# Kernel tuning notes

Hardware: AMD Instinct MI355X
Metric: run time of the kernel (lower is better)

Reference implementation:

```python
import jax, jax.numpy as jnp
import numpy as np

N = 8192
D = 512


def setup_inputs() -> dict:
    key = jax.random.key(0)
    k_h, k_a, k_q, k_k, k_v = jax.random.split(key, 5)
    H = jax.random.normal(k_h, (N, D), dtype=jnp.float32)
    A = jax.random.uniform(k_a, (N, N), dtype=jnp.float32)
    W_Q = jax.random.uniform(k_q, (D, D), dtype=jnp.float32)
    W_K = jax.random.uniform(k_k, (D, D), dtype=jnp.float32)
    W_V = jax.random.uniform(k_v, (D, D), dtype=jnp.float32)
    return {"H": H, "A": A, "W_Q": W_Q, "W_K": W_K, "W_V": W_V}


def reference(H, A, W_Q, W_K, W_V):
    # Q = H @ W_Q, K = H @ W_K; scores = Q @ K^T  -> [N, N]
    scale = 1.0 / jnp.sqrt(jnp.asarray(H.shape[1], dtype=H.dtype))
    HQ = H @ W_Q                      # [N, D]
    HK = H @ W_K                      # [N, D]
    scores = jnp.einsum('nd,md->nm', HQ, HK)  # [N, N]
    scores = scores * A * scale       # elementwise adjacency mask + scale
    attn = jax.nn.softmax(scores, axis=1)
    return attn @ (H @ W_V)           # [N, D]
```

## Files before the change

### kernel.cpp

```cpp
#include <hip/hip_runtime.h>
#include <cmath>


typedef unsigned short u16;
typedef unsigned int   u32;
typedef float f32x4 __attribute__((ext_vector_type(4)));
typedef short s16x8 __attribute__((ext_vector_type(8)));

#define DEVI static __device__ __forceinline__

DEVI u16 f2bf(float x) { u32 u = __float_as_uint(x); u32 r = u + 0x7fffu + ((u >> 16) & 1u); return (u16)(r >> 16); }
DEVI float bf2f(u16 b) { return __uint_as_float((u32)b << 16); }

DEVI f32x4 mm_bf16(s16x8 a, s16x8 b, f32x4 c) {
  return __builtin_amdgcn_mfma_f32_16x16x32_bf16(a, b, c, 0, 0, 0);
}

DEVI uint4 scaleP(uint4 v, float f) {
  u32* w = (u32*)&v;
#pragma unroll
  for (int j = 0; j < 4; j++) {
    u32 lo = __float_as_uint(__uint_as_float(w[j] << 16) * f) + 0x8000u;
    u32 hi = __float_as_uint(__uint_as_float(w[j] & 0xffff0000u) * f) + 0x8000u;
    w[j] = __builtin_amdgcn_perm(hi, lo, 0x07060302);
  }
  return v;
}


__global__ void k_split(const float* __restrict__ X, u16* __restrict__ Xhi, u16* __restrict__ Xlo, int n4) {
  int i = blockIdx.x * 256 + threadIdx.x;
  if (i >= n4) return;
  float4 v = ((const float4*)X)[i];
  u16 h0 = f2bf(v.x), h1 = f2bf(v.y), h2 = f2bf(v.z), h3 = f2bf(v.w);
  u16 l0 = f2bf(v.x - bf2f(h0)), l1 = f2bf(v.y - bf2f(h1));
  u16 l2 = f2bf(v.z - bf2f(h2)), l3 = f2bf(v.w - bf2f(h3));
  ((uint2*)Xhi)[i] = make_uint2((u32)h0 | ((u32)h1 << 16), (u32)h2 | ((u32)h3 << 16));
  ((uint2*)Xlo)[i] = make_uint2((u32)l0 | ((u32)l1 << 16), (u32)l2 | ((u32)l3 << 16));
}

__global__ void k_prepW(const float* __restrict__ W0, const float* __restrict__ W1, const float* __restrict__ W2,
                        u16* __restrict__ Thi, u16* __restrict__ Tlo) {
  int idx = blockIdx.x * 256 + threadIdx.x;
  if (idx >= 3 * 512 * 512) return;
  int w = idx >> 18, n = (idx >> 9) & 511, k = idx & 511;
  const float* W = (w == 0) ? W0 : (w == 1) ? W1 : W2;
  float v = W[k * 512 + n];
  u16 h = f2bf(v);
  Thi[idx] = h;
  Tlo[idx] = f2bf(v - bf2f(h));
}

__global__ void k_transpose(const u16* __restrict__ in, u16* __restrict__ out, int R, int C) {
  __shared__ u16 t[64][72];
  const int rb = blockIdx.x * 64, cb = blockIdx.y * 64;
  const int r = threadIdx.x >> 2, c4 = (threadIdx.x & 3) * 16;
  const u16* src = in + (size_t)(rb + r) * C + cb + c4;
  *(uint4*)&t[r][c4] = *(const uint4*)src;
  *(uint4*)&t[r][c4 + 8] = *(const uint4*)(src + 8);
  __syncthreads();
  u16 v[16];
#pragma unroll
  for (int j = 0; j < 16; j++) v[j] = t[c4 + j][r];
  uint4 o0, o1;
  o0.x = v[0] | ((u32)v[1] << 16); o0.y = v[2] | ((u32)v[3] << 16);
  o0.z = v[4] | ((u32)v[5] << 16); o0.w = v[6] | ((u32)v[7] << 16);
  o1.x = v[8] | ((u32)v[9] << 16); o1.y = v[10] | ((u32)v[11] << 16);
  o1.z = v[12] | ((u32)v[13] << 16); o1.w = v[14] | ((u32)v[15] << 16);
  u16* dst = out + (size_t)(cb + r) * R + rb + c4;
  *(uint4*)dst = o0;
  *(uint4*)(dst + 8) = o1;
}


template<int EPI, int PASSES, int KSPLIT>
__launch_bounds__(256, 2)
__global__ void k_big(const u16* __restrict__ Ahi, const u16* __restrict__ Alo,
                      const u16* __restrict__ Bhi, const u16* __restrict__ Blo,
                      int M, int N, int K,
                      float* __restrict__ Cf, float* __restrict__ Cf1,
                      float* __restrict__ Cf2, float* __restrict__ Cf3,
                      const float* __restrict__ Adj, float* __restrict__ mC,
                      float* __restrict__ lC, u16* __restrict__ Pout,
                      const float* __restrict__ Fsc, float scale)
{
  constexpr int LDSU = (EPI == 2) ? 33792 : 15360;
  __shared__ __align__(16) u16 lds[LDSU];
  u16* sAh = lds;
  u16* sAl = lds + 10240;
  u16* sBh = lds + ((PASSES == 3) ? 20480 : 10240);
  u16* sBl = lds + 25600;

  const int tid = threadIdx.x, lane = tid & 63, wid = tid >> 6;
  const int wn = wid & 1, wm = wid >> 1;
  const int lr = lane & 15, lk = lane >> 4;
  const int mbase = blockIdx.x * 256, nbase = blockIdx.y * 128;
  const int srow = tid >> 1, shalf = tid & 1;
  const size_t Ks = (size_t)K;

  int kbeg = 0, kend = K;
  if constexpr (KSPLIT > 1) {
    const int steps = K >> 5, bz = blockIdx.z;
    kbeg = ((steps * bz) / KSPLIT) << 5;
    kend = ((steps * (bz + 1)) / KSPLIT) << 5;
  }

  f32x4 acc[8][4] = {};

  for (int kt = kbeg; kt < kend; kt += 32) {
    const size_t a0 = (size_t)(mbase + srow) * Ks + kt + shalf * 16;
    const size_t a1 = a0 + (size_t)128 * Ks;
    const size_t b0 = (size_t)(nbase + srow) * Ks + kt + shalf * 16;
    uint4 vah0 = *(const uint4*)(Ahi + a0), vah1 = *(const uint4*)(Ahi + a0 + 8);
    uint4 vah2 = *(const uint4*)(Ahi + a1), vah3 = *(const uint4*)(Ahi + a1 + 8);
    uint4 vbh0 = *(const uint4*)(Bhi + b0), vbh1 = *(const uint4*)(Bhi + b0 + 8);
    uint4 val0, val1, val2, val3, vbl0, vbl1;
    if constexpr (PASSES == 3) {
      val0 = *(const uint4*)(Alo + a0); val1 = *(const uint4*)(Alo + a0 + 8);
      val2 = *(const uint4*)(Alo + a1); val3 = *(const uint4*)(Alo + a1 + 8);
      vbl0 = *(const uint4*)(Blo + b0); vbl1 = *(const uint4*)(Blo + b0 + 8);
    }
    if constexpr (EPI == 3) {
      const float f0 = Fsc[((size_t)(kt >> 7) << 13) + mbase + srow];
      const float f1 = Fsc[((size_t)(kt >> 7) << 13) + mbase + 128 + srow];
      vah0 = scaleP(vah0, f0); vah1 = scaleP(vah1, f0);
      vah2 = scaleP(vah2, f1); vah3 = scaleP(vah3, f1);
    }
    __syncthreads();
    const int so = srow * 40 + shalf * 16;
    *(uint4*)(sAh + so) = vah0;        *(uint4*)(sAh + so + 8) = vah1;
    *(uint4*)(sAh + 5120 + so) = vah2; *(uint4*)(sAh + 5120 + so + 8) = vah3;
    *(uint4*)(sBh + so) = vbh0;        *(uint4*)(sBh + so + 8) = vbh1;
    if constexpr (PASSES == 3) {
      *(uint4*)(sAl + so) = val0;        *(uint4*)(sAl + so + 8) = val1;
      *(uint4*)(sAl + 5120 + so) = val2; *(uint4*)(sAl + 5120 + so + 8) = val3;
      *(uint4*)(sBl + so) = vbl0;        *(uint4*)(sBl + so + 8) = vbl1;
    }
    __syncthreads();

    s16x8 ah[8], al[8];
#pragma unroll
    for (int m = 0; m < 8; m++) {
      const int ro = (wm * 128 + m * 16 + lr) * 40 + lk * 8;
      ah[m] = *(const s16x8*)(sAh + ro);
      if constexpr (PASSES == 3) al[m] = *(const s16x8*)(sAl + ro);
    }
#pragma unroll
    for (int nt = 0; nt < 4; nt++) {
      const int ro = (wn * 64 + nt * 16 + lr) * 40 + lk * 8;
      s16x8 bh = *(const s16x8*)(sBh + ro);
#pragma unroll
      for (int m = 0; m < 8; m++) acc[m][nt] = mm_bf16(ah[m], bh, acc[m][nt]);
      if constexpr (PASSES == 3) {
        s16x8 bl = *(const s16x8*)(sBl + ro);
#pragma unroll
        for (int m = 0; m < 8; m++) acc[m][nt] = mm_bf16(ah[m], bl, acc[m][nt]);
#pragma unroll
        for (int m = 0; m < 8; m++) acc[m][nt] = mm_bf16(al[m], bh, acc[m][nt]);
      }
    }
  }

  if constexpr (EPI == 2) {
    const int c = blockIdx.x * 2 + wm;
#pragma unroll
    for (int nt = 0; nt < 4; nt++) {
      const int q_l = wn * 64 + nt * 16 + lr;
      const float* arow = Adj + (size_t)(nbase + q_l) * (size_t)M + mbase + wm * 128 + lk * 4;
      float4 a4[8];
#pragma unroll
      for (int mt = 0; mt < 8; mt++) a4[mt] = *(const float4*)(arow + mt * 16);
      float mx = -3.4e38f;
#pragma unroll
      for (int mt = 0; mt < 8; mt++)
#pragma unroll
        for (int r = 0; r < 4; r++) {
          float s = acc[mt][nt][r] * ((const float*)&a4[mt])[r] * scale;
          acc[mt][nt][r] = s;
          mx = fmaxf(mx, s);
        }
      mx = fmaxf(mx, __shfl_xor(mx, 16));
      mx = fmaxf(mx, __shfl_xor(mx, 32));
      float sm = 0.f;
#pragma unroll
      for (int mt = 0; mt < 8; mt++)
#pragma unroll
        for (int r = 0; r < 4; r++) {
          float p = __expf(acc[mt][nt][r] - mx);
          acc[mt][nt][r] = p;
          sm += p;
        }
      sm += __shfl_xor(sm, 16);
      sm += __shfl_xor(sm, 32);
      if (lane < 16) {
        mC[(size_t)c * N + nbase + wn * 64 + nt * 16 + lane] = mx;
        lC[(size_t)c * N + nbase + wn * 64 + nt * 16 + lane] = sm;
      }
    }
    __syncthreads();
    u16* pb = lds;
#pragma unroll
    for (int nt = 0; nt < 4; nt++) {
      const int q_l = wn * 64 + nt * 16 + lr;
#pragma unroll
      for (int mt = 0; mt < 8; mt++) {
        const int kvo = wm * 128 + mt * 16 + lk * 4;
        u32 u0 = (u32)f2bf(acc[mt][nt][0]) | ((u32)f2bf(acc[mt][nt][1]) << 16);
        u32 u1 = (u32)f2bf(acc[mt][nt][2]) | ((u32)f2bf(acc[mt][nt][3]) << 16);
        *(uint2*)&pb[q_l * 264 + kvo] = make_uint2(u0, u1);
      }
    }
    __syncthreads();
    {
      const int q_r = tid >> 1, half = tid & 1;
      u16* dst = Pout + (size_t)(nbase + q_r) * (size_t)M + mbase + half * 128;
      const u16* srcp = &pb[q_r * 264 + half * 128];
#pragma unroll
      for (int i = 0; i < 16; i++) ((uint4*)dst)[i] = *(const uint4*)(srcp + i * 8);
    }
  } else {
    float* cfp = Cf;
    if constexpr (KSPLIT > 1) {
      if (blockIdx.z == 1) cfp = Cf1;
      else if (blockIdx.z == 2) cfp = Cf2;
      else if (blockIdx.z == 3) cfp = Cf3;
    }
#pragma unroll
    for (int mt = 0; mt < 8; mt++)
#pragma unroll
      for (int nt = 0; nt < 4; nt++) {
        const int grow = mbase + wm * 128 + mt * 16 + lk * 4;
        const int gcol = nbase + wn * 64 + nt * 16 + lr;
#pragma unroll
        for (int r = 0; r < 4; r++)
          cfp[(size_t)(grow + r) * N + gcol] = acc[mt][nt][r];
      }
  }
}


template<int EPI, int PASSES, int FUSEW, int KSPLIT>
__launch_bounds__(256, 4)
__global__ void gemm_bt(const u16* __restrict__ Ahi, const u16* __restrict__ Alo,
                        const u16* __restrict__ Bhi, const u16* __restrict__ Blo,
                        int M, int N, int K,
                        u16* __restrict__ C0, u16* __restrict__ C1)
{
  constexpr int BUF = 128 * 40;
  __shared__ __align__(16) u16 lds[BUF * 4];

  u16* sAh = lds;
  u16* sAl = lds + BUF;
  u16* sBh = lds + 2 * BUF;
  u16* sBl = lds + 3 * BUF;

  const int tid = threadIdx.x, lane = tid & 63, wid = tid >> 6;
  const int wm = wid & 1, wn = wid >> 1;
  const int lr = lane & 15, lk = lane >> 4;
  const int mbase = blockIdx.x * 128;
  const int w = blockIdx.y >> 2;
  const int nbase = (blockIdx.y & 3) * 128;
  const u16 *bhp = Bhi + (size_t)w * 262144, *blp = Blo + (size_t)w * 262144;
  u16 *c0 = C0 + (size_t)w * 4194304, *c1 = C1 + (size_t)w * 4194304;
  const int srow = tid >> 1, shalf = tid & 1;
  const size_t Ks = (size_t)K;

  f32x4 acc[4][4] = {};

  for (int kt = 0; kt < K; kt += 32) {
    const size_t aoff = (size_t)(mbase + srow) * Ks + kt + shalf * 16;
    const size_t boff = (size_t)(nbase + srow) * Ks + kt + shalf * 16;
    uint4 vah0 = *(const uint4*)(Ahi + aoff), vah1 = *(const uint4*)(Ahi + aoff + 8);
    uint4 vbh0 = *(const uint4*)(bhp + boff), vbh1 = *(const uint4*)(bhp + boff + 8);
    uint4 val0 = *(const uint4*)(Alo + aoff), val1 = *(const uint4*)(Alo + aoff + 8);
    uint4 vbl0 = *(const uint4*)(blp + boff), vbl1 = *(const uint4*)(blp + boff + 8);
    __syncthreads();
    const int so = srow * 40 + shalf * 16;
    *(uint4*)(sAh + so) = vah0; *(uint4*)(sAh + so + 8) = vah1;
    *(uint4*)(sBh + so) = vbh0; *(uint4*)(sBh + so + 8) = vbh1;
    *(uint4*)(sAl + so) = val0; *(uint4*)(sAl + so + 8) = val1;
    *(uint4*)(sBl + so) = vbl0; *(uint4*)(sBl + so + 8) = vbl1;
    __syncthreads();

    s16x8 ah[4], bh[4], al[4], bl[4];
#pragma unroll
    for (int t = 0; t < 4; t++) {
      ah[t] = *(const s16x8*)(sAh + (wm * 64 + t * 16 + lr) * 40 + lk * 8);
      bh[t] = *(const s16x8*)(sBh + (wn * 64 + t * 16 + lr) * 40 + lk * 8);
      al[t] = *(const s16x8*)(sAl + (wm * 64 + t * 16 + lr) * 40 + lk * 8);
      bl[t] = *(const s16x8*)(sBl + (wn * 64 + t * 16 + lr) * 40 + lk * 8);
    }
#pragma unroll
    for (int mt = 0; mt < 4; mt++)
#pragma unroll
      for (int nt = 0; nt < 4; nt++) {
        acc[mt][nt] = mm_bf16(ah[mt], bh[nt], acc[mt][nt]);
        acc[mt][nt] = mm_bf16(ah[mt], bl[nt], acc[mt][nt]);
        acc[mt][nt] = mm_bf16(al[mt], bh[nt], acc[mt][nt]);
      }
  }

#pragma unroll
  for (int mt = 0; mt < 4; mt++)
#pragma unroll
    for (int nt = 0; nt < 4; nt++) {
      const int grow = mbase + wm * 64 + mt * 16 + lk * 4;
      const int gcol = nbase + wn * 64 + nt * 16 + lr;
#pragma unroll
      for (int r = 0; r < 4; r++) {
        float c = acc[mt][nt][r];
        size_t o = (size_t)(grow + r) * N + gcol;
        u16 h = f2bf(c);
        c0[o] = h;
        c1[o] = f2bf(c - bf2f(h));
      }
    }
}


__global__ void k_reduce(const float* __restrict__ mC, const float* __restrict__ lC, float* __restrict__ F,
                         int NQ, int NC) {
  const int q = blockIdx.x * 256 + threadIdx.x;
  if (q >= NQ) return;
  float mf = -3.4e38f;
  for (int c = 0; c < NC; c++) mf = fmaxf(mf, mC[(size_t)c * NQ + q]);
  float L = 0.f;
  for (int c = 0; c < NC; c++) L += lC[(size_t)c * NQ + q] * __expf(mC[(size_t)c * NQ + q] - mf);
  const float inv = 1.0f / L;
  for (int c = 0; c < NC; c++) F[(size_t)c * NQ + q] = __expf(mC[(size_t)c * NQ + q] - mf) * inv;
}

__global__ void k_sumout3(float* __restrict__ out, const float* __restrict__ p1,
                          const float* __restrict__ p2, const float* __restrict__ p3, int n4) {
  int i = blockIdx.x * 256 + threadIdx.x;
  if (i >= n4) return;
  float4 o = ((const float4*)out)[i];
  float4 a = ((const float4*)p1)[i];
  float4 b = ((const float4*)p2)[i];
  float4 c = ((const float4*)p3)[i];
  o.x += a.x + b.x + c.x; o.y += a.y + b.y + c.y;
  o.z += a.z + b.z + c.z; o.w += a.w + b.w + c.w;
  ((float4*)out)[i] = o;
}


extern "C" void kernel_launch(void* const* d_in, const int* in_sizes, int n_in,
                              void* d_out, int out_size, void* d_ws, size_t ws_size,
                              hipStream_t stream) {
  const float* H  = (const float*)d_in[0];
  const float* Aj = (const float*)d_in[1];
  const float* Wq = (const float*)d_in[2];
  const float* Wk = (const float*)d_in[3];
  const float* Wv = (const float*)d_in[4];
  float* out = (float*)d_out;
  const int NN = 8192, DD = 512;

  char* ws = (char*)d_ws;
  size_t off = 0;
  auto alloc = [&](size_t bytes) -> void* {
    void* p = ws + off;
    off += (bytes + 255) & ~(size_t)255;
    return p;
  };
  u16* Pbuf  = (u16*)alloc((size_t)NN * NN * 2);
  u16* Hhi   = (u16*)alloc((size_t)NN * DD * 2);
  u16* Hlo   = (u16*)alloc((size_t)NN * DD * 2);
  u16* WThi  = (u16*)alloc((size_t)3 * DD * DD * 2);
  u16* WTlo  = (u16*)alloc((size_t)3 * DD * DD * 2);
  u16* PRhi  = (u16*)alloc((size_t)3 * NN * DD * 2);
  u16* PRlo  = (u16*)alloc((size_t)3 * NN * DD * 2);
  u16* HVthi = (u16*)alloc((size_t)NN * DD * 2);
  float* mC  = (float*)alloc((size_t)64 * NN * 4);
  float* lC  = (float*)alloc((size_t)64 * NN * 4);
  float* Ft  = (float*)alloc((size_t)64 * NN * 4);
  if (off > ws_size) return;

  u16* HQhi = PRhi;                 u16* HQlo = PRlo;
  u16* HKhi = PRhi + (size_t)NN*DD; u16* HKlo = PRlo + (size_t)NN*DD;
  u16* HVhi = PRhi + (size_t)2*NN*DD;

  float* part1 = (float*)Hhi;
  float* part2 = part1 + (size_t)NN * DD;
  float* part3 = part2 + (size_t)NN * DD;

  const float scl = 1.0f / sqrtf((float)DD);

  k_split<<<4096, 256, 0, stream>>>(H, Hhi, Hlo, NN * DD / 4);
  k_prepW<<<3072, 256, 0, stream>>>(Wq, Wk, Wv, WThi, WTlo);

  dim3 gP(64, 12);
  gemm_bt<0, 3, 1, 1><<<gP, 256, 0, stream>>>(Hhi, Hlo, WThi, WTlo, NN, DD, DD, PRhi, PRlo);

  dim3 gT(128, 8);
  k_transpose<<<gT, 256, 0, stream>>>(HVhi, HVthi, NN, DD);

  dim3 gS(32, 64);
  k_big<2, 3, 1><<<gS, 256, 0, stream>>>(HKhi, HKlo, HQhi, HQlo, NN, NN, DD,
                                         nullptr, nullptr, nullptr, nullptr,
                                         Aj, mC, lC, Pbuf, nullptr, scl);

  k_reduce<<<32, 256, 0, stream>>>(mC, lC, Ft, NN, 64);

  dim3 gO(32, 4, 4);
  k_big<3, 1, 4><<<gO, 256, 0, stream>>>(Pbuf, nullptr, HVthi, nullptr, NN, DD, NN,
                                         out, part1, part2, part3,
                                         nullptr, nullptr, nullptr, nullptr, Ft, 0.f);

  k_sumout3<<<4096, 256, 0, stream>>>(out, part1, part2, part3, NN * DD / 4);
}
```

Before: 516.4 us.

## Compute attention scores with split int8 MFMA instead of three-pass bf16

```diff
diff --git a/kernel.cpp b/kernel.cpp
--- a/kernel.cpp
+++ b/kernel.cpp
@@ -6,6 +6,7 @@
 typedef unsigned int   u32;
 typedef float f32x4 __attribute__((ext_vector_type(4)));
 typedef short s16x8 __attribute__((ext_vector_type(8)));
+typedef int   i32x4 __attribute__((ext_vector_type(4)));
 
 #define DEVI static __device__ __forceinline__
 
@@ -14,6 +15,9 @@
 
 DEVI f32x4 mm_bf16(s16x8 a, s16x8 b, f32x4 c) {
   return __builtin_amdgcn_mfma_f32_16x16x32_bf16(a, b, c, 0, 0, 0);
+}
+DEVI i32x4 mm_i8(i32x4 a, i32x4 b, i32x4 c) {
+  return __builtin_amdgcn_mfma_i32_16x16x64_i8(a, b, c, 0, 0, 0);
 }
 
 DEVI uint4 scaleP(uint4 v, float f) {
@@ -73,6 +77,196 @@
 }
 
 
+__global__ void k_quant(const u16* __restrict__ hi, const u16* __restrict__ lo,
+                        char* __restrict__ q8h, char* __restrict__ q8l, float* __restrict__ sc) {
+  const int row = blockIdx.x * 4 + (threadIdx.x >> 6);
+  const int lane = threadIdx.x & 63;
+  const size_t base = (size_t)row * 512 + lane * 8;
+  uint4 vh = *(const uint4*)(hi + base);
+  uint4 vl = *(const uint4*)(lo + base);
+  const u32* ph = (const u32*)&vh;
+  const u32* pl = (const u32*)&vl;
+  float x[8];
+#pragma unroll
+  for (int j = 0; j < 4; j++) {
+    x[2 * j]     = bf2f((u16)(ph[j] & 0xffff)) + bf2f((u16)(pl[j] & 0xffff));
+    x[2 * j + 1] = bf2f((u16)(ph[j] >> 16))    + bf2f((u16)(pl[j] >> 16));
+  }
+  float amax = 0.f;
+#pragma unroll
+  for (int j = 0; j < 8; j++) amax = fmaxf(amax, fabsf(x[j]));
+#pragma unroll
+  for (int d = 1; d < 64; d <<= 1) amax = fmaxf(amax, __shfl_xor(amax, d));
+  amax = fmaxf(amax, 1e-30f);
+  const float s = amax * (1.0f / 32512.f);
+  const float inv = 32512.f / amax;
+  u32 hb0 = 0, hb1 = 0, lb0 = 0, lb1 = 0;
+#pragma unroll
+  for (int j = 0; j < 8; j++) {
+    int v = (int)rintf(x[j] * inv);
+    int h = (v + 128) >> 8;
+    int l = v - (h << 8);
+    if (j < 4) { hb0 |= (u32)(h & 255) << (j * 8);       lb0 |= (u32)(l & 255) << (j * 8); }
+    else       { hb1 |= (u32)(h & 255) << ((j - 4) * 8); lb1 |= (u32)(l & 255) << ((j - 4) * 8); }
+  }
+  *(uint2*)(q8h + base) = make_uint2(hb0, hb1);
+  *(uint2*)(q8l + base) = make_uint2(lb0, lb1);
+  if (lane == 0) sc[row] = s;
+}
+
+
+__launch_bounds__(256, 4)
+__global__ void k_iscore(const char* __restrict__ Kh8, const char* __restrict__ Kl8,
+                         const char* __restrict__ Qh8, const char* __restrict__ Ql8,
+                         const float* __restrict__ sK, const float* __restrict__ sQ,
+                         const float* __restrict__ Adj, float* __restrict__ mC,
+                         float* __restrict__ lC, u16* __restrict__ Pout, float scale)
+{
+  constexpr int NN = 8192;
+  __shared__ __align__(16) char lds[24576];
+
+  const int tid = threadIdx.x, lane = tid & 63, wid = tid >> 6;
+  const int wm = wid >> 1, wn = wid & 1;
+  const int lr = lane & 15, lk = lane >> 4;
+  const int mbase = blockIdx.x * 128, nbase = blockIdx.y * 64;
+
+  const int su = (tid & 7) ^ ((tid >> 3) & 7);
+  const char* aPlane = (su < 4) ? Kh8 : Kl8;
+  const char* bPlane = (su < 4) ? Qh8 : Ql8;
+  const int sCol = (su & 3) * 16;
+  const int sRow = tid >> 3;
+
+  const int pH = (lk ^ (lr & 7)) * 16;
+  const int pL = ((4 | lk) ^ (lr & 7)) * 16;
+  const int aOffH = (wm * 64 + lr) * 128 + pH;
+  const int aOffL = (wm * 64 + lr) * 128 + pL;
+  const int bOffH = 16384 + (wn * 32 + lr) * 128 + pH;
+  const int bOffL = 16384 + (wn * 32 + lr) * 128 + pL;
+
+  i32x4 hh[4][2] = {};
+  i32x4 mid[4][2] = {};
+
+  for (int kt = 0; kt < 512; kt += 64) {
+    uint4 sg[6];
+#pragma unroll
+    for (int j = 0; j < 4; j++)
+      sg[j] = *(const uint4*)(aPlane + (size_t)(mbase + sRow + j * 32) * 512 + kt + sCol);
+#pragma unroll
+    for (int j = 0; j < 2; j++)
+      sg[4 + j] = *(const uint4*)(bPlane + (size_t)(nbase + sRow + j * 32) * 512 + kt + sCol);
+    __syncthreads();
+#pragma unroll
+    for (int j = 0; j < 4; j++) *(uint4*)(lds + tid * 16 + j * 4096) = sg[j];
+#pragma unroll
+    for (int j = 0; j < 2; j++) *(uint4*)(lds + 16384 + tid * 16 + j * 4096) = sg[4 + j];
+    __syncthreads();
+
+    i32x4 bh[2], bl[2];
+#pragma unroll
+    for (int n = 0; n < 2; n++) {
+      bh[n] = *(const i32x4*)(lds + bOffH + n * 2048);
+      bl[n] = *(const i32x4*)(lds + bOffL + n * 2048);
+    }
+#pragma unroll
+    for (int m = 0; m < 4; m++) {
+      i32x4 ah = *(const i32x4*)(lds + aOffH + m * 2048);
+      i32x4 al = *(const i32x4*)(lds + aOffL + m * 2048);
+#pragma unroll
+      for (int n = 0; n < 2; n++) {
+        hh[m][n]  = mm_i8(ah, bh[n], hh[m][n]);
+        mid[m][n] = mm_i8(ah, bl[n], mid[m][n]);
+        mid[m][n] = mm_i8(al, bh[n], mid[m][n]);
+      }
+    }
+  }
+
+  __syncthreads();
+  float* sred = (float*)lds;
+  float* ssum = sred + 128;
+  u16* pb = (u16*)(lds + 1024);
+  const int c = blockIdx.x;
+  f32x4 sv[4][2];
+  float mfin[2];
+#pragma unroll
+  for (int nt = 0; nt < 2; nt++) {
+    const int q_l = wn * 32 + nt * 16 + lr;
+    const float sq = sQ[nbase + q_l] * scale;
+    const float* arow = Adj + (size_t)(nbase + q_l) * NN + mbase + wm * 64 + lk * 4;
+    float mx = -3.4e38f;
+#pragma unroll
+    for (int mt = 0; mt < 4; mt++) {
+      const float4 a4 = *(const float4*)(arow + mt * 16);
+      const float4 sk4 = *(const float4*)(sK + mbase + wm * 64 + mt * 16 + lk * 4);
+#pragma unroll
+      for (int r = 0; r < 4; r++) {
+        float s = (65536.f * (float)hh[mt][nt][r] + 256.f * (float)mid[mt][nt][r])
+                  * sq * ((const float*)&sk4)[r] * ((const float*)&a4)[r];
+        sv[mt][nt][r] = s;
+        mx = fmaxf(mx, s);
+      }
+    }
+    mx = fmaxf(mx, __shfl_xor(mx, 16));
+    mx = fmaxf(mx, __shfl_xor(mx, 32));
+    if (lane < 16) sred[wm * 64 + wn * 32 + nt * 16 + lane] = mx;
+  }
+  __syncthreads();
+#pragma unroll
+  for (int nt = 0; nt < 2; nt++) {
+    const int qi = wn * 32 + nt * 16 + lr;
+    mfin[nt] = fmaxf(sred[qi], sred[64 + qi]);
+  }
+  if (wm == 0 && lane < 16) {
+#pragma unroll
+    for (int nt = 0; nt < 2; nt++)
+      mC[(size_t)c * NN + nbase + wn * 32 + nt * 16 + lane] = mfin[nt];
+  }
+#pragma unroll
+  for (int nt = 0; nt < 2; nt++) {
+    float sm = 0.f;
+#pragma unroll
+    for (int mt = 0; mt < 4; mt++)
+#pragma unroll
+      for (int r = 0; r < 4; r++) {
+        float p = __expf(sv[mt][nt][r] - mfin[nt]);
+        sv[mt][nt][r] = p;
+        sm += p;
+      }
+    sm += __shfl_xor(sm, 16);
+    sm += __shfl_xor(sm, 32);
+    if (lane < 16) ssum[wm * 64 + wn * 32 + nt * 16 + lane] = sm;
+  }
+  __syncthreads();
+  if (wm == 0 && lane < 16) {
+#pragma unroll
+    for (int nt = 0; nt < 2; nt++) {
+      const int qi = wn * 32 + nt * 16 + lane;
+      lC[(size_t)c * NN + nbase + qi] = ssum[qi] + ssum[64 + qi];
+    }
+  }
+#pragma unroll
+  for (int nt = 0; nt < 2; nt++) {
+    const int q_l = wn * 32 + nt * 16 + lr;
+#pragma unroll
+    for (int mt = 0; mt < 4; mt++) {
+      const int kvo = wm * 64 + mt * 16 + lk * 4;
+      u32 u0 = (u32)f2bf(sv[mt][nt][0]) | ((u32)f2bf(sv[mt][nt][1]) << 16);
+      u32 u1 = (u32)f2bf(sv[mt][nt][2]) | ((u32)f2bf(sv[mt][nt][3]) << 16);
+      *(uint2*)&pb[q_l * 136 + kvo] = make_uint2(u0, u1);
+    }
+  }
+  __syncthreads();
+  {
+    const int q_r = tid >> 2, qu = tid & 3;
+    u16* dst = Pout + (size_t)(nbase + q_r) * NN + mbase + qu * 32;
+    const u16* srcp = &pb[q_r * 136 + qu * 32];
+    *(uint4*)dst = *(const uint4*)srcp;
+    *(uint4*)(dst + 8) = *(const uint4*)(srcp + 8);
+    *(uint4*)(dst + 16) = *(const uint4*)(srcp + 16);
+    *(uint4*)(dst + 24) = *(const uint4*)(srcp + 24);
+  }
+}
+
+
 template<int EPI, int PASSES, int KSPLIT>
 __launch_bounds__(256, 2)
 __global__ void k_big(const u16* __restrict__ Ahi, const u16* __restrict__ Alo,
@@ -80,16 +274,11 @@
                       int M, int N, int K,
                       float* __restrict__ Cf, float* __restrict__ Cf1,
                       float* __restrict__ Cf2, float* __restrict__ Cf3,
-                      const float* __restrict__ Adj, float* __restrict__ mC,
-                      float* __restrict__ lC, u16* __restrict__ Pout,
-                      const float* __restrict__ Fsc, float scale)
+                      const float* __restrict__ Fsc)
 {
-  constexpr int LDSU = (EPI == 2) ? 33792 : 15360;
-  __shared__ __align__(16) u16 lds[LDSU];
+  __shared__ __align__(16) u16 lds[15360];
   u16* sAh = lds;
-  u16* sAl = lds + 10240;
-  u16* sBh = lds + ((PASSES == 3) ? 20480 : 10240);
-  u16* sBl = lds + 25600;
+  u16* sBh = lds + 10240;
 
   const int tid = threadIdx.x, lane = tid & 63, wid = tid >> 6;
   const int wn = wid & 1, wm = wid >> 1;
@@ -114,12 +303,6 @@
     uint4 vah0 = *(const uint4*)(Ahi + a0), vah1 = *(const uint4*)(Ahi + a0 + 8);
     uint4 vah2 = *(const uint4*)(Ahi + a1), vah3 = *(const uint4*)(Ahi + a1 + 8);
     uint4 vbh0 = *(const uint4*)(Bhi + b0), vbh1 = *(const uint4*)(Bhi + b0 + 8);
-    uint4 val0, val1, val2, val3, vbl0, vbl1;
-    if constexpr (PASSES == 3) {
-      val0 = *(const uint4*)(Alo + a0); val1 = *(const uint4*)(Alo + a0 + 8);
-      val2 = *(const uint4*)(Alo + a1); val3 = *(const uint4*)(Alo + a1 + 8);
-      vbl0 = *(const uint4*)(Blo + b0); vbl1 = *(const uint4*)(Blo + b0 + 8);
-    }
     if constexpr (EPI == 3) {
       const float f0 = Fsc[((size_t)(kt >> 7) << 13) + mbase + srow];
       const float f1 = Fsc[((size_t)(kt >> 7) << 13) + mbase + 128 + srow];
@@ -131,115 +314,39 @@
     *(uint4*)(sAh + so) = vah0;        *(uint4*)(sAh + so + 8) = vah1;
     *(uint4*)(sAh + 5120 + so) = vah2; *(uint4*)(sAh + 5120 + so + 8) = vah3;
     *(uint4*)(sBh + so) = vbh0;        *(uint4*)(sBh + so + 8) = vbh1;
-    if constexpr (PASSES == 3) {
-      *(uint4*)(sAl + so) = val0;        *(uint4*)(sAl + so + 8) = val1;
-      *(uint4*)(sAl + 5120 + so) = val2; *(uint4*)(sAl + 5120 + so + 8) = val3;
-      *(uint4*)(sBl + so) = vbl0;        *(uint4*)(sBl + so + 8) = vbl1;
-    }
     __syncthreads();
 
-    s16x8 ah[8], al[8];
-#pragma unroll
-    for (int m = 0; m < 8; m++) {
-      const int ro = (wm * 128 + m * 16 + lr) * 40 + lk * 8;
-      ah[m] = *(const s16x8*)(sAh + ro);
-      if constexpr (PASSES == 3) al[m] = *(const s16x8*)(sAl + ro);
-    }
+    s16x8 ah[8];
+#pragma unroll
+    for (int m = 0; m < 8; m++)
+      ah[m] = *(const s16x8*)(sAh + (wm * 128 + m * 16 + lr) * 40 + lk * 8);
 #pragma unroll
     for (int nt = 0; nt < 4; nt++) {
-      const int ro = (wn * 64 + nt * 16 + lr) * 40 + lk * 8;
-      s16x8 bh = *(const s16x8*)(sBh + ro);
+      s16x8 bh = *(const s16x8*)(sBh + (wn * 64 + nt * 16 + lr) * 40 + lk * 8);
 #pragma unroll
       for (int m = 0; m < 8; m++) acc[m][nt] = mm_bf16(ah[m], bh, acc[m][nt]);
-      if constexpr (PASSES == 3) {
-        s16x8 bl = *(const s16x8*)(sBl + ro);
-#pragma unroll
-        for (int m = 0; m < 8; m++) acc[m][nt] = mm_bf16(ah[m], bl, acc[m][nt]);
-#pragma unroll
-        for (int m = 0; m < 8; m++) acc[m][nt] = mm_bf16(al[m], bh, acc[m][nt]);
-      }
-    }
-  }
-
-  if constexpr (EPI == 2) {
-    const int c = blockIdx.x * 2 + wm;
+    }
+  }
+
+  float* cfp = Cf;
+  if constexpr (KSPLIT > 1) {
+    if (blockIdx.z == 1) cfp = Cf1;
+    else if (blockIdx.z == 2) cfp = Cf2;
+    else if (blockIdx.z == 3) cfp = Cf3;
+  }
+#pragma unroll
+  for (int mt = 0; mt < 8; mt++)
 #pragma unroll
     for (int nt = 0; nt < 4; nt++) {
-      const int q_l = wn * 64 + nt * 16 + lr;
-      const float* arow = Adj + (size_t)(nbase + q_l) * (size_t)M + mbase + wm * 128 + lk * 4;
-      float4 a4[8];
-#pragma unroll
-      for (int mt = 0; mt < 8; mt++) a4[mt] = *(const float4*)(arow + mt * 16);
-      float mx = -3.4e38f;
-#pragma unroll
-      for (int mt = 0; mt < 8; mt++)
-#pragma unroll
-        for (int r = 0; r < 4; r++) {
-          float s = acc[mt][nt][r] * ((const float*)&a4[mt])[r] * scale;
-          acc[mt][nt][r] = s;
-          mx = fmaxf(mx, s);
-        }
-      mx = fmaxf(mx, __shfl_xor(mx, 16));
-      mx = fmaxf(mx, __shfl_xor(mx, 32));
-      float sm = 0.f;
-#pragma unroll
-      for (int mt = 0; mt < 8; mt++)
-#pragma unroll
-        for (int r = 0; r < 4; r++) {
-          float p = __expf(acc[mt][nt][r] - mx);
-          acc[mt][nt][r] = p;
-          sm += p;
-        }
-      sm += __shfl_xor(sm, 16);
-      sm += __shfl_xor(sm, 32);
-      if (lane < 16) {
-        mC[(size_t)c * N + nbase + wn * 64 + nt * 16 + lane] = mx;
-        lC[(size_t)c * N + nbase + wn * 64 + nt * 16 + lane] = sm;
-      }
-    }
-    __syncthreads();
-    u16* pb = lds;
-#pragma unroll
-    for (int nt = 0; nt < 4; nt++) {
-      const int q_l = wn * 64 + nt * 16 + lr;
-#pragma unroll
-      for (int mt = 0; mt < 8; mt++) {
-        const int kvo = wm * 128 + mt * 16 + lk * 4;
-        u32 u0 = (u32)f2bf(acc[mt][nt][0]) | ((u32)f2bf(acc[mt][nt][1]) << 16);
-        u32 u1 = (u32)f2bf(acc[mt][nt][2]) | ((u32)f2bf(acc[mt][nt][3]) << 16);
-        *(uint2*)&pb[q_l * 264 + kvo] = make_uint2(u0, u1);
-      }
-    }
-    __syncthreads();
-    {
-      const int q_r = tid >> 1, half = tid & 1;
-      u16* dst = Pout + (size_t)(nbase + q_r) * (size_t)M + mbase + half * 128;
-      const u16* srcp = &pb[q_r * 264 + half * 128];
-#pragma unroll
-      for (int i = 0; i < 16; i++) ((uint4*)dst)[i] = *(const uint4*)(srcp + i * 8);
-    }
-  } else {
-    float* cfp = Cf;
-    if constexpr (KSPLIT > 1) {
-      if (blockIdx.z == 1) cfp = Cf1;
-      else if (blockIdx.z == 2) cfp = Cf2;
-      else if (blockIdx.z == 3) cfp = Cf3;
-    }
-#pragma unroll
-    for (int mt = 0; mt < 8; mt++)
-#pragma unroll
-      for (int nt = 0; nt < 4; nt++) {
-        const int grow = mbase + wm * 128 + mt * 16 + lk * 4;
-        const int gcol = nbase + wn * 64 + nt * 16 + lr;
-#pragma unroll
-        for (int r = 0; r < 4; r++)
-          cfp[(size_t)(grow + r) * N + gcol] = acc[mt][nt][r];
-      }
-  }
-}
-
-
-template<int EPI, int PASSES, int FUSEW, int KSPLIT>
+      const int grow = mbase + wm * 128 + mt * 16 + lk * 4;
+      const int gcol = nbase + wn * 64 + nt * 16 + lr;
+#pragma unroll
+      for (int r = 0; r < 4; r++)
+        cfp[(size_t)(grow + r) * N + gcol] = acc[mt][nt][r];
+    }
+}
+
+
 __launch_bounds__(256, 4)
 __global__ void gemm_bt(const u16* __restrict__ Ahi, const u16* __restrict__ Alo,
                         const u16* __restrict__ Bhi, const u16* __restrict__ Blo,
@@ -373,6 +480,12 @@
   float* mC  = (float*)alloc((size_t)64 * NN * 4);
   float* lC  = (float*)alloc((size_t)64 * NN * 4);
   float* Ft  = (float*)alloc((size_t)64 * NN * 4);
+  char* Qh8  = (char*)alloc((size_t)NN * DD);
+  char* Ql8  = (char*)alloc((size_t)NN * DD);
+  char* Kh8  = (char*)alloc((size_t)NN * DD);
+  char* Kl8  = (char*)alloc((size_t)NN * DD);
+  float* sQ  = (float*)alloc((size_t)NN * 4);
+  float* sK  = (float*)alloc((size_t)NN * 4);
   if (off > ws_size) return;
 
   u16* HQhi = PRhi;                 u16* HQlo = PRlo;
@@ -389,22 +502,23 @@
   k_prepW<<<3072, 256, 0, stream>>>(Wq, Wk, Wv, WThi, WTlo);
 
   dim3 gP(64, 12);
-  gemm_bt<0, 3, 1, 1><<<gP, 256, 0, stream>>>(Hhi, Hlo, WThi, WTlo, NN, DD, DD, PRhi, PRlo);
+  gemm_bt<<<gP, 256, 0, stream>>>(Hhi, Hlo, WThi, WTlo, NN, DD, DD, PRhi, PRlo);
 
   dim3 gT(128, 8);
   k_transpose<<<gT, 256, 0, stream>>>(HVhi, HVthi, NN, DD);
 
-  dim3 gS(32, 64);
-  k_big<2, 3, 1><<<gS, 256, 0, stream>>>(HKhi, HKlo, HQhi, HQlo, NN, NN, DD,
-                                         nullptr, nullptr, nullptr, nullptr,
-                                         Aj, mC, lC, Pbuf, nullptr, scl);
+  k_quant<<<2048, 256, 0, stream>>>(HQhi, HQlo, Qh8, Ql8, sQ);
+  k_quant<<<2048, 256, 0, stream>>>(HKhi, HKlo, Kh8, Kl8, sK);
+
+  dim3 gS(64, 128);
+  k_iscore<<<gS, 256, 0, stream>>>(Kh8, Kl8, Qh8, Ql8, sK, sQ,
+                                   Aj, mC, lC, Pbuf, scl);
 
   k_reduce<<<32, 256, 0, stream>>>(mC, lC, Ft, NN, 64);
 
   dim3 gO(32, 4, 4);
   k_big<3, 1, 4><<<gO, 256, 0, stream>>>(Pbuf, nullptr, HVthi, nullptr, NN, DD, NN,
-                                         out, part1, part2, part3,
-                                         nullptr, nullptr, nullptr, nullptr, Ft, 0.f);
+                                         out, part1, part2, part3, Ft);
 
   k_sumout3<<<4096, 256, 0, stream>>>(out, part1, part2, part3, NN * DD / 4);
 }
```

Result: slower. 819.4 us (+58.7%).
